# Kernel tuning notes

Hardware: AMD Instinct MI355X
Metric: run time of the kernel (lower is better)

## Reference

```python
import jax, jax.numpy as jnp
import numpy as np

N_NODES = 100000
N_EDGES = 1000000
IN_DIM = 64
HID = 64
OUT = 64
NEG_SLOPE = 0.2  # PyG GATConv default


def setup_inputs() -> dict:
    key = jax.random.key(0)
    ks = jax.random.split(key, 10)
    x = jax.random.normal(ks[0], (N_NODES, IN_DIM), dtype=jnp.float32)
    edge_index = jax.random.randint(ks[1], (2, N_EDGES), 0, N_NODES, dtype=jnp.int64)
    s = 1.0 / np.sqrt(IN_DIM)
    sh = 1.0 / np.sqrt(HID)
    W_src = jax.random.uniform(ks[2], (IN_DIM, HID), jnp.float32, -s, s)
    W_dst = jax.random.uniform(ks[3], (IN_DIM, HID), jnp.float32, -s, s)
    att_src = jax.random.uniform(ks[4], (HID,), jnp.float32, -sh, sh)
    att_dst = jax.random.uniform(ks[5], (HID,), jnp.float32, -sh, sh)
    bias = jnp.zeros((HID,), jnp.float32)
    W_lin = jax.random.uniform(ks[6], (HID, OUT), jnp.float32, -sh, sh)
    b_lin = jax.random.uniform(ks[7], (OUT,), jnp.float32, -sh, sh)
    return {"x": x, "edge_index": edge_index, "W_src": W_src, "W_dst": W_dst,
            "att_src": att_src, "att_dst": att_dst, "bias": bias,
            "W_lin": W_lin, "b_lin": b_lin}


def reference(x, edge_index, W_src, W_dst, att_src, att_dst, bias, W_lin, b_lin):
    src, tgt = edge_index[0], edge_index[1]
    # Bias-free linear projections (PyG GATConv with tuple in_channels)
    h_src = x @ W_src                      # [N, HID]
    h_dst = x @ W_dst                      # [N, HID]
    a_src = h_src @ att_src                # [N]
    a_dst = h_dst @ att_dst                # [N]
    # Per-edge attention logits: LeakyReLU(a_src[j] + a_dst[i])
    e = a_src[src] + a_dst[tgt]            # [E]
    e = jnp.where(e > 0, e, NEG_SLOPE * e)
    # Segment-softmax over incoming edges of each target node
    seg_max = jax.ops.segment_max(e, tgt, num_segments=N_NODES)  # [N]
    expw = jnp.exp(e - seg_max[tgt])                             # [E]
    denom = jax.ops.segment_sum(expw, tgt, num_segments=N_NODES)  # [N]
    alpha = expw / (denom[tgt] + 1e-16)                          # [E]
    # Scatter-aggregate weighted source features
    msgs = alpha[:, None] * h_src[src]                           # [E, HID]
    out = jax.ops.segment_sum(msgs, tgt, num_segments=N_NODES)   # [N, HID]
    out = out + bias
    # Final linear + ReLU
    return jax.nn.relu(out @ W_lin + b_lin)
```

## Files before the change

### kernel.cpp

```cpp
#include <hip/hip_runtime.h>
#include <hip/hip_fp16.h>
#include <math.h>

#define HID 64
#define CBITS 6
#define CSZ 64
#define MAXB 2048
#define CAP 832
#define PB 896
#define MSB 256
#define XSTR 17

__device__ __forceinline__ float4 f4fma(float a, const float4 b, float4 c) {
    c.x = fmaf(a, b.x, c.x); c.y = fmaf(a, b.y, c.y);
    c.z = fmaf(a, b.z, c.z); c.w = fmaf(a, b.w, c.w);
    return c;
}

__global__ void __launch_bounds__(256)
mid_kernel(const float* __restrict__ x,
           const float* __restrict__ W_src,
           const float* __restrict__ W_dst,
           const float* __restrict__ att_src,
           const float* __restrict__ att_dst,
           __half* __restrict__ h_half,
           float* __restrict__ a_src,
           float* __restrict__ a_dst, int N,
           const int* __restrict__ src, const int* __restrict__ tgt,
           int* __restrict__ gcursor, int* __restrict__ rec, int E, int nbc) {
    __shared__ __align__(16) char smraw[25600];
    const int t = threadIdx.x;

    if (blockIdx.x < PB) {
        float4* Ws4  = (float4*)smraw;
        float4* att4 = Ws4 + HID * 16;
        float4* vd4  = att4 + 16;
        float4* xs4f = vd4 + 16;

        for (int i = t; i < HID * 16; i += 256) Ws4[i] = ((const float4*)W_src)[i];
        if (t < 16) att4[t] = ((const float4*)att_src)[t];
        if (t < HID) {
            float acc = 0.0f;
#pragma unroll 8
            for (int h = 0; h < HID; ++h)
                acc = fmaf(W_dst[t * HID + h], att_dst[h], acc);
            ((float*)vd4)[t] = acc;
        }

        const int g0 = t >> 4;
        const int s = t & 15;
        const float4* x4 = (const float4*)x;
        uint2* h2 = (uint2*)h_half;

        for (int base = blockIdx.x * 32; base < N; base += PB * 32) {
            __syncthreads();
#pragma unroll
            for (int u = 0; u < 2; ++u) {
                int f = t + u * 256;
                int node = base + (f >> 4);
                xs4f[(f >> 4) * XSTR + (f & 15)] =
                    (node < N) ? x4[(long long)node * 16 + (f & 15)]
                               : make_float4(0, 0, 0, 0);
            }
            __syncthreads();

            const float4* xr0 = xs4f + g0 * XSTR;
            const float4* xr1 = xs4f + (g0 + 16) * XSTR;

            float4 acc0 = make_float4(0, 0, 0, 0);
            float4 acc1 = make_float4(0, 0, 0, 0);
#pragma unroll 4
            for (int kk = 0; kk < 16; ++kk) {
                float4 xv0 = xr0[kk];
                float4 xv1 = xr1[kk];
                float4 w0 = Ws4[(4 * kk + 0) * 16 + s];
                float4 w1 = Ws4[(4 * kk + 1) * 16 + s];
                float4 w2 = Ws4[(4 * kk + 2) * 16 + s];
                float4 w3 = Ws4[(4 * kk + 3) * 16 + s];
                acc0 = f4fma(xv0.x, w0, acc0);
                acc1 = f4fma(xv1.x, w0, acc1);
                acc0 = f4fma(xv0.y, w1, acc0);
                acc1 = f4fma(xv1.y, w1, acc1);
                acc0 = f4fma(xv0.z, w2, acc0);
                acc1 = f4fma(xv1.z, w2, acc1);
                acc0 = f4fma(xv0.w, w3, acc0);
                acc1 = f4fma(xv1.w, w3, acc1);
            }

            float4 av = att4[s], qv = vd4[s];
            float p0 = acc0.x * av.x + acc0.y * av.y + acc0.z * av.z + acc0.w * av.w;
            float p1 = acc1.x * av.x + acc1.y * av.y + acc1.z * av.z + acc1.w * av.w;
            float4 xq0 = xr0[s];
            float4 xq1 = xr1[s];
            float q0 = xq0.x * qv.x + xq0.y * qv.y + xq0.z * qv.z + xq0.w * qv.w;
            float q1 = xq1.x * qv.x + xq1.y * qv.y + xq1.z * qv.z + xq1.w * qv.w;
#pragma unroll
            for (int off = 1; off < 16; off <<= 1) {
                p0 += __shfl_xor(p0, off, 64);
                p1 += __shfl_xor(p1, off, 64);
                q0 += __shfl_xor(q0, off, 64);
                q1 += __shfl_xor(q1, off, 64);
            }

            int n0 = base + g0, n1 = base + g0 + 16;
            if (n0 < N) {
                __half2 lo = __float22half2_rn(make_float2(acc0.x, acc0.y));
                __half2 hi = __float22half2_rn(make_float2(acc0.z, acc0.w));
                uint2 pk; pk.x = *(unsigned*)&lo; pk.y = *(unsigned*)&hi;
                h2[(long long)n0 * 16 + s] = pk;
                if (s == 0) { a_src[n0] = p0; a_dst[n0] = q0; }
            }
            if (n1 < N) {
                __half2 lo = __float22half2_rn(make_float2(acc1.x, acc1.y));
                __half2 hi = __float22half2_rn(make_float2(acc1.z, acc1.w));
                uint2 pk; pk.x = *(unsigned*)&lo; pk.y = *(unsigned*)&hi;
                h2[(long long)n1 * 16 + s] = pk;
                if (s == 0) { a_src[n1] = p1; a_dst[n1] = q1; }
            }
        }
    } else {
        int* lh = (int*)smraw;
        const int bid = blockIdx.x - PB;

        for (int i = t; i < nbc; i += 256) lh[i] = 0;
        __syncthreads();
        int chunk = (E + MSB - 1) / MSB;
        int e0 = bid * chunk;
        int e1 = min(E, e0 + chunk);
        for (int e = e0 + t; e < e1; e += 256)
            atomicAdd(&lh[tgt[e] >> CBITS], 1);
        __syncthreads();
        for (int i = t; i < nbc; i += 256)
            if (lh[i]) lh[i] = i * CAP + atomicAdd(&gcursor[i], lh[i]);
        __syncthreads();
        for (int e = e0 + t; e < e1; e += 256) {
            int s = src[e], tg = tgt[e];
            int bi = tg >> CBITS;
            int pos = atomicAdd(&lh[bi], 1);
            if (pos < (bi + 1) * CAP)
                rec[pos] = (s << CBITS) | (tg & (CSZ - 1));
        }
    }
}

__global__ void __launch_bounds__(256)
sort_gather_kernel(const int* __restrict__ gcursor, const int* __restrict__ rec,
                   const __half* __restrict__ h_half,
                   const float* __restrict__ a_src, const float* __restrict__ a_dst,
                   const float* __restrict__ bias,
                   const float* __restrict__ W_lin, const float* __restrict__ b_lin,
                   float* __restrict__ out, int N) {
    __shared__ float4 Wl4[HID * 16];
    __shared__ float4 bs4[16], bl4[16];
    __shared__ int ssort[CAP];
    __shared__ int hist[CSZ];
    __shared__ int loff[CSZ + 1];
    __shared__ int cur[CSZ];

    const int t = threadIdx.x;
    for (int i = t; i < HID * 16; i += 256) Wl4[i] = ((const float4*)W_lin)[i];
    if (t < 16) {
        bs4[t] = ((const float4*)bias)[t];
        bl4[t] = ((const float4*)b_lin)[t];
    }

    const int bk = blockIdx.x;
    const int node0 = bk << CBITS;
    const int nn = min(CSZ, N - node0);
    const int beg = bk * CAP;
    int cnt = gcursor[bk];
    if (cnt > CAP) cnt = CAP;

    if (t < CSZ) hist[t] = 0;
    __syncthreads();
    for (int j = t; j < cnt; j += 256)
        atomicAdd(&hist[rec[beg + j] & (CSZ - 1)], 1);
    __syncthreads();
    if (t < CSZ) {
        int h = hist[t];
        int v = h;
#pragma unroll
        for (int off = 1; off < CSZ; off <<= 1) {
            int u = __shfl_up(v, off, 64);
            if (t >= off) v += u;
        }
        loff[t] = v - h;
        cur[t]  = v - h;
        if (t == CSZ - 1) loff[CSZ] = v;
    }
    __syncthreads();
    for (int j = t; j < cnt; j += 256) {
        int r = rec[beg + j];
        int pos = atomicAdd(&cur[r & (CSZ - 1)], 1);
        ssort[pos] = r >> CBITS;
    }
    __syncthreads();

    const int lane = t & 63;
    const int w = t >> 6;
    const int g = lane >> 4;
    const int s = lane & 15;
    const int gbase = g << 4;
    const uint2* h2 = (const uint2*)h_half;
    float4* out4 = (float4*)out;

#pragma unroll 1
    for (int r2 = 0; r2 < 4; ++r2) {
        int nloc = w * 16 + r2 * 4 + g;
        int n = node0 + nloc;
        bool act = (nloc < nn);
        float adn = act ? a_dst[n] : 0.0f;
        int jb = loff[nloc];
        int je = loff[nloc + 1];

        float4 acc = make_float4(0, 0, 0, 0);
        float dsum = 0.0f;
        int j = jb;
        for (; j + 4 <= je; j += 4) {
            int s0 = ssort[j], s1 = ssort[j + 1], s2 = ssort[j + 2], s3 = ssort[j + 3];
            uint2 r0 = h2[(long long)s0 * 16 + s];
            uint2 r1 = h2[(long long)s1 * 16 + s];
            uint2 r2v = h2[(long long)s2 * 16 + s];
            uint2 r3 = h2[(long long)s3 * 16 + s];
            float v0 = a_src[s0] + adn, v1 = a_src[s1] + adn;
            float v2 = a_src[s2] + adn, v3 = a_src[s3] + adn;
            v0 = (v0 > 0.0f) ? v0 : 0.2f * v0;
            v1 = (v1 > 0.0f) ? v1 : 0.2f * v1;
            v2 = (v2 > 0.0f) ? v2 : 0.2f * v2;
            v3 = (v3 > 0.0f) ? v3 : 0.2f * v3;
            float w0 = __expf(v0), w1 = __expf(v1);
            float w2 = __expf(v2), w3 = __expf(v3);
            dsum += (w0 + w1) + (w2 + w3);
            float2 f0a = __half22float2(*(const __half2*)&r0.x);
            float2 f0b = __half22float2(*(const __half2*)&r0.y);
            float2 f1a = __half22float2(*(const __half2*)&r1.x);
            float2 f1b = __half22float2(*(const __half2*)&r1.y);
            float2 f2a = __half22float2(*(const __half2*)&r2v.x);
            float2 f2b = __half22float2(*(const __half2*)&r2v.y);
            float2 f3a = __half22float2(*(const __half2*)&r3.x);
            float2 f3b = __half22float2(*(const __half2*)&r3.y);
            acc.x = fmaf(w0, f0a.x, fmaf(w1, f1a.x, fmaf(w2, f2a.x, fmaf(w3, f3a.x, acc.x))));
            acc.y = fmaf(w0, f0a.y, fmaf(w1, f1a.y, fmaf(w2, f2a.y, fmaf(w3, f3a.y, acc.y))));
            acc.z = fmaf(w0, f0b.x, fmaf(w1, f1b.x, fmaf(w2, f2b.x, fmaf(w3, f3b.x, acc.z))));
            acc.w = fmaf(w0, f0b.y, fmaf(w1, f1b.y, fmaf(w2, f2b.y, fmaf(w3, f3b.y, acc.w))));
        }
        for (; j < je; ++j) {
            int s0 = ssort[j];
            uint2 r0 = h2[(long long)s0 * 16 + s];
            float v0 = a_src[s0] + adn;
            v0 = (v0 > 0.0f) ? v0 : 0.2f * v0;
            float w0 = __expf(v0);
            dsum += w0;
            float2 f0a = __half22float2(*(const __half2*)&r0.x);
            float2 f0b = __half22float2(*(const __half2*)&r0.y);
            acc.x = fmaf(w0, f0a.x, acc.x);
            acc.y = fmaf(w0, f0a.y, acc.y);
            acc.z = fmaf(w0, f0b.x, acc.z);
            acc.w = fmaf(w0, f0b.y, acc.w);
        }

        float inv = 1.0f / (dsum + 1e-16f);
        float4 bsv = bs4[s];
        float4 r;
        r.x = fmaf(acc.x, inv, bsv.x);
        r.y = fmaf(acc.y, inv, bsv.y);
        r.z = fmaf(acc.z, inv, bsv.z);
        r.w = fmaf(acc.w, inv, bsv.w);

        float4 o = bl4[s];
#pragma unroll 4
        for (int ks = 0; ks < 16; ++ks) {
            float rx = __shfl(r.x, gbase + ks, 64);
            float ry = __shfl(r.y, gbase + ks, 64);
            float rz = __shfl(r.z, gbase + ks, 64);
            float rw = __shfl(r.w, gbase + ks, 64);
            o = f4fma(rx, Wl4[(4 * ks + 0) * 16 + s], o);
            o = f4fma(ry, Wl4[(4 * ks + 1) * 16 + s], o);
            o = f4fma(rz, Wl4[(4 * ks + 2) * 16 + s], o);
            o = f4fma(rw, Wl4[(4 * ks + 3) * 16 + s], o);
        }

        if (act) {
            float4 res;
            res.x = o.x > 0.0f ? o.x : 0.0f;
            res.y = o.y > 0.0f ? o.y : 0.0f;
            res.z = o.z > 0.0f ? o.z : 0.0f;
            res.w = o.w > 0.0f ? o.w : 0.0f;
            out4[(long long)n * 16 + s] = res;
        }
    }
}

extern "C" void kernel_launch(void* const* d_in, const int* in_sizes, int n_in,
                              void* d_out, int out_size, void* d_ws, size_t ws_size,
                              hipStream_t stream) {
    const float* x       = (const float*)d_in[0];
    const int*   edge    = (const int*)d_in[1];
    const float* W_src   = (const float*)d_in[2];
    const float* W_dst   = (const float*)d_in[3];
    const float* att_src = (const float*)d_in[4];
    const float* att_dst = (const float*)d_in[5];
    const float* bias    = (const float*)d_in[6];
    const float* W_lin   = (const float*)d_in[7];
    const float* b_lin   = (const float*)d_in[8];
    float* out = (float*)d_out;

    const int N = in_sizes[0] / HID;
    const int E = in_sizes[1] / 2;
    const int* src = edge;
    const int* tgt = edge + E;
    const int nbc = (N + CSZ - 1) / CSZ;

    __half* h_half  = (__half*)d_ws;
    float*  a_src   = (float*)(h_half + (size_t)N * HID);
    float*  a_dst   = a_src + N;
    int*    gcursor = (int*)(a_dst + N);
    int*    rec     = gcursor + MAXB;

    hipMemsetAsync(gcursor, 0, MAXB * sizeof(int), stream);
    mid_kernel<<<PB + MSB, 256, 0, stream>>>(x, W_src, W_dst, att_src, att_dst,
                                             h_half, a_src, a_dst, N,
                                             src, tgt, gcursor, rec, E, nbc);
    sort_gather_kernel<<<nbc, 256, 0, stream>>>(gcursor, rec, h_half, a_src, a_dst,
                                                bias, W_lin, b_lin, out, N);
}
```

Before: 166.9 us.

## Software-pipeline gather loop, keep records in registers, init cursors via kernel

The gather loop now prefetches the next four source rows and attention scores while it computes on the current four, hiding load latency. The bucket records are loaded once into registers and reused for both the histogram and the scatter passes instead of being reread from global memory. Bias vectors move from shared memory into registers, launch bounds request 8 waves' occupancy, and the memset is replaced by a small kernel that seeds each cursor with its bucket base offset. The risks are higher register pressure from the prefetch buffers and a hard-coded cap of four records per thread, which assumes CAP is at most 1024.

Measured after the change: 165.3 us. About the same (-1.0%).

```diff
diff --git a/kernel.cpp b/kernel.cpp
--- a/kernel.cpp
+++ b/kernel.cpp
@@ -15,6 +15,12 @@
     c.x = fmaf(a, b.x, c.x); c.y = fmaf(a, b.y, c.y);
     c.z = fmaf(a, b.z, c.z); c.w = fmaf(a, b.w, c.w);
     return c;
+}
+
+__global__ void init_kernel(int* __restrict__ gcursor, int nbc) {
+    int stride = gridDim.x * blockDim.x;
+    for (int i = blockIdx.x * blockDim.x + threadIdx.x; i < nbc; i += stride)
+        gcursor[i] = i * CAP;
 }
 
 __global__ void __launch_bounds__(256)
@@ -131,7 +137,7 @@
             atomicAdd(&lh[tgt[e] >> CBITS], 1);
         __syncthreads();
         for (int i = t; i < nbc; i += 256)
-            if (lh[i]) lh[i] = i * CAP + atomicAdd(&gcursor[i], lh[i]);
+            if (lh[i]) lh[i] = atomicAdd(&gcursor[i], lh[i]);
         __syncthreads();
         for (int e = e0 + t; e < e1; e += 256) {
             int s = src[e], tg = tgt[e];
@@ -143,7 +149,7 @@
     }
 }
 
-__global__ void __launch_bounds__(256)
+__global__ void __launch_bounds__(256, 8)
 sort_gather_kernel(const int* __restrict__ gcursor, const int* __restrict__ rec,
                    const __half* __restrict__ h_half,
                    const float* __restrict__ a_src, const float* __restrict__ a_dst,
@@ -151,30 +157,31 @@
                    const float* __restrict__ W_lin, const float* __restrict__ b_lin,
                    float* __restrict__ out, int N) {
     __shared__ float4 Wl4[HID * 16];
-    __shared__ float4 bs4[16], bl4[16];
-    __shared__ int ssort[CAP];
-    __shared__ int hist[CSZ];
-    __shared__ int loff[CSZ + 1];
-    __shared__ int cur[CSZ];
+    __shared__ int   ssort[CAP];
+    __shared__ int   loff[CSZ + 1];
+    __shared__ int   hist[CSZ];
 
     const int t = threadIdx.x;
     for (int i = t; i < HID * 16; i += 256) Wl4[i] = ((const float4*)W_lin)[i];
-    if (t < 16) {
-        bs4[t] = ((const float4*)bias)[t];
-        bl4[t] = ((const float4*)b_lin)[t];
-    }
 
     const int bk = blockIdx.x;
     const int node0 = bk << CBITS;
     const int nn = min(CSZ, N - node0);
     const int beg = bk * CAP;
-    int cnt = gcursor[bk];
+    int cnt = gcursor[bk] - beg;
     if (cnt > CAP) cnt = CAP;
 
     if (t < CSZ) hist[t] = 0;
     __syncthreads();
-    for (int j = t; j < cnt; j += 256)
-        atomicAdd(&hist[rec[beg + j] & (CSZ - 1)], 1);
+
+    int q0 = (t       < cnt) ? rec[beg + t      ] : -1;
+    int q1 = (t + 256 < cnt) ? rec[beg + t + 256] : -1;
+    int q2 = (t + 512 < cnt) ? rec[beg + t + 512] : -1;
+    int q3 = (t + 768 < cnt) ? rec[beg + t + 768] : -1;
+    if (q0 >= 0) atomicAdd(&hist[q0 & (CSZ - 1)], 1);
+    if (q1 >= 0) atomicAdd(&hist[q1 & (CSZ - 1)], 1);
+    if (q2 >= 0) atomicAdd(&hist[q2 & (CSZ - 1)], 1);
+    if (q3 >= 0) atomicAdd(&hist[q3 & (CSZ - 1)], 1);
     __syncthreads();
     if (t < CSZ) {
         int h = hist[t];
@@ -185,15 +192,14 @@
             if (t >= off) v += u;
         }
         loff[t] = v - h;
-        cur[t]  = v - h;
+        hist[t] = v - h;
         if (t == CSZ - 1) loff[CSZ] = v;
     }
     __syncthreads();
-    for (int j = t; j < cnt; j += 256) {
-        int r = rec[beg + j];
-        int pos = atomicAdd(&cur[r & (CSZ - 1)], 1);
-        ssort[pos] = r >> CBITS;
-    }
+    if (q0 >= 0) ssort[atomicAdd(&hist[q0 & (CSZ - 1)], 1)] = q0;
+    if (q1 >= 0) ssort[atomicAdd(&hist[q1 & (CSZ - 1)], 1)] = q1;
+    if (q2 >= 0) ssort[atomicAdd(&hist[q2 & (CSZ - 1)], 1)] = q2;
+    if (q3 >= 0) ssort[atomicAdd(&hist[q3 & (CSZ - 1)], 1)] = q3;
     __syncthreads();
 
     const int lane = t & 63;
@@ -203,6 +209,8 @@
     const int gbase = g << 4;
     const uint2* h2 = (const uint2*)h_half;
     float4* out4 = (float4*)out;
+    const float4 bsv = ((const float4*)bias)[s];
+    const float4 blv = ((const float4*)b_lin)[s];
 
 #pragma unroll 1
     for (int r2 = 0; r2 < 4; ++r2) {
@@ -216,14 +224,28 @@
         float4 acc = make_float4(0, 0, 0, 0);
         float dsum = 0.0f;
         int j = jb;
-        for (; j + 4 <= je; j += 4) {
-            int s0 = ssort[j], s1 = ssort[j + 1], s2 = ssort[j + 2], s3 = ssort[j + 3];
-            uint2 r0 = h2[(long long)s0 * 16 + s];
-            uint2 r1 = h2[(long long)s1 * 16 + s];
-            uint2 r2v = h2[(long long)s2 * 16 + s];
-            uint2 r3 = h2[(long long)s3 * 16 + s];
-            float v0 = a_src[s0] + adn, v1 = a_src[s1] + adn;
-            float v2 = a_src[s2] + adn, v3 = a_src[s3] + adn;
+        uint2 pr0 = make_uint2(0, 0), pr1 = pr0, pr2 = pr0, pr3 = pr0;
+        float pa0 = 0.0f, pa1 = 0.0f, pa2 = 0.0f, pa3 = 0.0f;
+        if (j + 4 <= je) {
+            int c0 = ssort[j] >> CBITS,     c1 = ssort[j + 1] >> CBITS;
+            int c2 = ssort[j + 2] >> CBITS, c3 = ssort[j + 3] >> CBITS;
+            pr0 = h2[((unsigned)c0 << 4) + s];
+            pr1 = h2[((unsigned)c1 << 4) + s];
+            pr2 = h2[((unsigned)c2 << 4) + s];
+            pr3 = h2[((unsigned)c3 << 4) + s];
+            pa0 = a_src[c0]; pa1 = a_src[c1]; pa2 = a_src[c2]; pa3 = a_src[c3];
+        }
+#pragma unroll 1
+        for (; j + 8 <= je; j += 4) {
+            int c0 = ssort[j + 4] >> CBITS, c1 = ssort[j + 5] >> CBITS;
+            int c2 = ssort[j + 6] >> CBITS, c3 = ssort[j + 7] >> CBITS;
+            uint2 nr0 = h2[((unsigned)c0 << 4) + s];
+            uint2 nr1 = h2[((unsigned)c1 << 4) + s];
+            uint2 nr2 = h2[((unsigned)c2 << 4) + s];
+            uint2 nr3 = h2[((unsigned)c3 << 4) + s];
+            float na0 = a_src[c0], na1 = a_src[c1];
+            float na2 = a_src[c2], na3 = a_src[c3];
+            float v0 = pa0 + adn, v1 = pa1 + adn, v2 = pa2 + adn, v3 = pa3 + adn;
             v0 = (v0 > 0.0f) ? v0 : 0.2f * v0;
             v1 = (v1 > 0.0f) ? v1 : 0.2f * v1;
             v2 = (v2 > 0.0f) ? v2 : 0.2f * v2;
@@ -231,23 +253,48 @@
             float w0 = __expf(v0), w1 = __expf(v1);
             float w2 = __expf(v2), w3 = __expf(v3);
             dsum += (w0 + w1) + (w2 + w3);
-            float2 f0a = __half22float2(*(const __half2*)&r0.x);
-            float2 f0b = __half22float2(*(const __half2*)&r0.y);
-            float2 f1a = __half22float2(*(const __half2*)&r1.x);
-            float2 f1b = __half22float2(*(const __half2*)&r1.y);
-            float2 f2a = __half22float2(*(const __half2*)&r2v.x);
-            float2 f2b = __half22float2(*(const __half2*)&r2v.y);
-            float2 f3a = __half22float2(*(const __half2*)&r3.x);
-            float2 f3b = __half22float2(*(const __half2*)&r3.y);
+            float2 f0a = __half22float2(*(const __half2*)&pr0.x);
+            float2 f0b = __half22float2(*(const __half2*)&pr0.y);
+            float2 f1a = __half22float2(*(const __half2*)&pr1.x);
+            float2 f1b = __half22float2(*(const __half2*)&pr1.y);
+            float2 f2a = __half22float2(*(const __half2*)&pr2.x);
+            float2 f2b = __half22float2(*(const __half2*)&pr2.y);
+            float2 f3a = __half22float2(*(const __half2*)&pr3.x);
+            float2 f3b = __half22float2(*(const __half2*)&pr3.y);
             acc.x = fmaf(w0, f0a.x, fmaf(w1, f1a.x, fmaf(w2, f2a.x, fmaf(w3, f3a.x, acc.x))));
             acc.y = fmaf(w0, f0a.y, fmaf(w1, f1a.y, fmaf(w2, f2a.y, fmaf(w3, f3a.y, acc.y))));
             acc.z = fmaf(w0, f0b.x, fmaf(w1, f1b.x, fmaf(w2, f2b.x, fmaf(w3, f3b.x, acc.z))));
             acc.w = fmaf(w0, f0b.y, fmaf(w1, f1b.y, fmaf(w2, f2b.y, fmaf(w3, f3b.y, acc.w))));
+            pr0 = nr0; pr1 = nr1; pr2 = nr2; pr3 = nr3;
+            pa0 = na0; pa1 = na1; pa2 = na2; pa3 = na3;
+        }
+        if (j + 4 <= je) {
+            float v0 = pa0 + adn, v1 = pa1 + adn, v2 = pa2 + adn, v3 = pa3 + adn;
+            v0 = (v0 > 0.0f) ? v0 : 0.2f * v0;
+            v1 = (v1 > 0.0f) ? v1 : 0.2f * v1;
+            v2 = (v2 > 0.0f) ? v2 : 0.2f * v2;
+            v3 = (v3 > 0.0f) ? v3 : 0.2f * v3;
+            float w0 = __expf(v0), w1 = __expf(v1);
+            float w2 = __expf(v2), w3 = __expf(v3);
+            dsum += (w0 + w1) + (w2 + w3);
+            float2 f0a = __half22float2(*(const __half2*)&pr0.x);
+            float2 f0b = __half22float2(*(const __half2*)&pr0.y);
+            float2 f1a = __half22float2(*(const __half2*)&pr1.x);
+            float2 f1b = __half22float2(*(const __half2*)&pr1.y);
+            float2 f2a = __half22float2(*(const __half2*)&pr2.x);
+            float2 f2b = __half22float2(*(const __half2*)&pr2.y);
+            float2 f3a = __half22float2(*(const __half2*)&pr3.x);
+            float2 f3b = __half22float2(*(const __half2*)&pr3.y);
+            acc.x = fmaf(w0, f0a.x, fmaf(w1, f1a.x, fmaf(w2, f2a.x, fmaf(w3, f3a.x, acc.x))));
+            acc.y = fmaf(w0, f0a.y, fmaf(w1, f1a.y, fmaf(w2, f2a.y, fmaf(w3, f3a.y, acc.y))));
+            acc.z = fmaf(w0, f0b.x, fmaf(w1, f1b.x, fmaf(w2, f2b.x, fmaf(w3, f3b.x, acc.z))));
+            acc.w = fmaf(w0, f0b.y, fmaf(w1, f1b.y, fmaf(w2, f2b.y, fmaf(w3, f3b.y, acc.w))));
+            j += 4;
         }
         for (; j < je; ++j) {
-            int s0 = ssort[j];
-            uint2 r0 = h2[(long long)s0 * 16 + s];
-            float v0 = a_src[s0] + adn;
+            int c0 = ssort[j] >> CBITS;
+            uint2 r0 = h2[((unsigned)c0 << 4) + s];
+            float v0 = a_src[c0] + adn;
             v0 = (v0 > 0.0f) ? v0 : 0.2f * v0;
             float w0 = __expf(v0);
             dsum += w0;
@@ -260,14 +307,13 @@
         }
 
         float inv = 1.0f / (dsum + 1e-16f);
-        float4 bsv = bs4[s];
         float4 r;
         r.x = fmaf(acc.x, inv, bsv.x);
         r.y = fmaf(acc.y, inv, bsv.y);
         r.z = fmaf(acc.z, inv, bsv.z);
         r.w = fmaf(acc.w, inv, bsv.w);
 
-        float4 o = bl4[s];
+        float4 o = blv;
 #pragma unroll 4
         for (int ks = 0; ks < 16; ++ks) {
             float rx = __shfl(r.x, gbase + ks, 64);
@@ -317,7 +363,7 @@
     int*    gcursor = (int*)(a_dst + N);
     int*    rec     = gcursor + MAXB;
 
-    hipMemsetAsync(gcursor, 0, MAXB * sizeof(int), stream);
+    init_kernel<<<8, 256, 0, stream>>>(gcursor, nbc);
     mid_kernel<<<PB + MSB, 256, 0, stream>>>(x, W_src, W_dst, att_src, att_dst,
                                              h_half, a_src, a_dst, N,
                                              src, tgt, gcursor, rec, E, nbc);
```

## Load x directly from global, precompute W_dst·att_dst in init kernel

Applied to the files above, without the earlier changes.

Replaces the hipMemsetAsync with a small init kernel that computes the W_dst·att_dst vector once and seeds each bucket cursor with its base offset (i*CAP), so the scatter and gather stages no longer add the base themselves. The projection blocks stop staging x tiles in LDS: each thread reads its x rows straight from global memory, which removes two __syncthreads per tile and shrinks shared memory for better occupancy. In exchange, the same x row is re-read by the 16 threads of a group through cache rather than from LDS.

New measurement: 179.3 us. 1.07x slower.

```diff
diff --git a/kernel.cpp b/kernel.cpp
--- a/kernel.cpp
+++ b/kernel.cpp
@@ -9,7 +9,6 @@
 #define CAP 832
 #define PB 896
 #define MSB 256
-#define XSTR 17
 
 __device__ __forceinline__ float4 f4fma(float a, const float4 b, float4 c) {
     c.x = fmaf(a, b.x, c.x); c.y = fmaf(a, b.y, c.y);
@@ -17,62 +16,64 @@
     return c;
 }
 
+__global__ void init_kernel(const float* __restrict__ W_dst,
+                            const float* __restrict__ att_dst,
+                            float* __restrict__ vdst,
+                            int* __restrict__ gcursor, int nbc) {
+    if (blockIdx.x == 0 && threadIdx.x < HID) {
+        int k = threadIdx.x;
+        float acc = 0.0f;
+#pragma unroll 8
+        for (int h = 0; h < HID; ++h) acc = fmaf(W_dst[k * HID + h], att_dst[h], acc);
+        vdst[k] = acc;
+    }
+    int stride = gridDim.x * blockDim.x;
+    for (int i = blockIdx.x * blockDim.x + threadIdx.x; i < nbc; i += stride)
+        gcursor[i] = i * CAP;
+}
+
 __global__ void __launch_bounds__(256)
 mid_kernel(const float* __restrict__ x,
            const float* __restrict__ W_src,
-           const float* __restrict__ W_dst,
            const float* __restrict__ att_src,
-           const float* __restrict__ att_dst,
+           const float* __restrict__ vdst,
            __half* __restrict__ h_half,
            float* __restrict__ a_src,
            float* __restrict__ a_dst, int N,
            const int* __restrict__ src, const int* __restrict__ tgt,
            int* __restrict__ gcursor, int* __restrict__ rec, int E, int nbc) {
-    __shared__ __align__(16) char smraw[25600];
+    __shared__ __align__(16) char smraw[16896];
     const int t = threadIdx.x;
 
     if (blockIdx.x < PB) {
         float4* Ws4  = (float4*)smraw;
         float4* att4 = Ws4 + HID * 16;
         float4* vd4  = att4 + 16;
-        float4* xs4f = vd4 + 16;
 
         for (int i = t; i < HID * 16; i += 256) Ws4[i] = ((const float4*)W_src)[i];
-        if (t < 16) att4[t] = ((const float4*)att_src)[t];
-        if (t < HID) {
-            float acc = 0.0f;
-#pragma unroll 8
-            for (int h = 0; h < HID; ++h)
-                acc = fmaf(W_dst[t * HID + h], att_dst[h], acc);
-            ((float*)vd4)[t] = acc;
-        }
+        if (t < 16) {
+            att4[t] = ((const float4*)att_src)[t];
+            vd4[t]  = ((const float4*)vdst)[t];
+        }
+        __syncthreads();
 
         const int g0 = t >> 4;
         const int s = t & 15;
         const float4* x4 = (const float4*)x;
         uint2* h2 = (uint2*)h_half;
+        const float4 zf4 = make_float4(0, 0, 0, 0);
 
         for (int base = blockIdx.x * 32; base < N; base += PB * 32) {
-            __syncthreads();
-#pragma unroll
-            for (int u = 0; u < 2; ++u) {
-                int f = t + u * 256;
-                int node = base + (f >> 4);
-                xs4f[(f >> 4) * XSTR + (f & 15)] =
-                    (node < N) ? x4[(long long)node * 16 + (f & 15)]
-                               : make_float4(0, 0, 0, 0);
-            }
-            __syncthreads();
-
-            const float4* xr0 = xs4f + g0 * XSTR;
-            const float4* xr1 = xs4f + (g0 + 16) * XSTR;
-
-            float4 acc0 = make_float4(0, 0, 0, 0);
-            float4 acc1 = make_float4(0, 0, 0, 0);
+            const int n0 = base + g0, n1 = base + g0 + 16;
+            const bool a0 = (n0 < N), a1 = (n1 < N);
+            const float4* xp0 = x4 + (long long)n0 * 16;
+            const float4* xp1 = x4 + (long long)n1 * 16;
+
+            float4 acc0 = zf4, acc1 = zf4;
 #pragma unroll 4
             for (int kk = 0; kk < 16; ++kk) {
-                float4 xv0 = xr0[kk];
-                float4 xv1 = xr1[kk];
+                float4 xv0 = a0 ? xp0[kk] : zf4;
+                float4 xv1 = a1 ? xp1[kk] : zf4;
                 float4 w0 = Ws4[(4 * kk + 0) * 16 + s];
                 float4 w1 = Ws4[(4 * kk + 1) * 16 + s];
                 float4 w2 = Ws4[(4 * kk + 2) * 16 + s];
@@ -90,8 +91,8 @@
             float4 av = att4[s], qv = vd4[s];
             float p0 = acc0.x * av.x + acc0.y * av.y + acc0.z * av.z + acc0.w * av.w;
             float p1 = acc1.x * av.x + acc1.y * av.y + acc1.z * av.z + acc1.w * av.w;
-            float4 xq0 = xr0[s];
-            float4 xq1 = xr1[s];
+            float4 xq0 = a0 ? xp0[s] : zf4;
+            float4 xq1 = a1 ? xp1[s] : zf4;
             float q0 = xq0.x * qv.x + xq0.y * qv.y + xq0.z * qv.z + xq0.w * qv.w;
             float q1 = xq1.x * qv.x + xq1.y * qv.y + xq1.z * qv.z + xq1.w * qv.w;
 #pragma unroll
@@ -102,15 +103,14 @@
                 q1 += __shfl_xor(q1, off, 64);
             }
 
-            int n0 = base + g0, n1 = base + g0 + 16;
-            if (n0 < N) {
+            if (a0) {
                 __half2 lo = __float22half2_rn(make_float2(acc0.x, acc0.y));
                 __half2 hi = __float22half2_rn(make_float2(acc0.z, acc0.w));
                 uint2 pk; pk.x = *(unsigned*)&lo; pk.y = *(unsigned*)&hi;
                 h2[(long long)n0 * 16 + s] = pk;
                 if (s == 0) { a_src[n0] = p0; a_dst[n0] = q0; }
             }
-            if (n1 < N) {
+            if (a1) {
                 __half2 lo = __float22half2_rn(make_float2(acc1.x, acc1.y));
                 __half2 hi = __float22half2_rn(make_float2(acc1.z, acc1.w));
                 uint2 pk; pk.x = *(unsigned*)&lo; pk.y = *(unsigned*)&hi;
@@ -131,7 +131,7 @@
             atomicAdd(&lh[tgt[e] >> CBITS], 1);
         __syncthreads();
         for (int i = t; i < nbc; i += 256)
-            if (lh[i]) lh[i] = i * CAP + atomicAdd(&gcursor[i], lh[i]);
+            if (lh[i]) lh[i] = atomicAdd(&gcursor[i], lh[i]);
         __syncthreads();
         for (int e = e0 + t; e < e1; e += 256) {
             int s = src[e], tg = tgt[e];
@@ -168,7 +168,7 @@
     const int node0 = bk << CBITS;
     const int nn = min(CSZ, N - node0);
     const int beg = bk * CAP;
-    int cnt = gcursor[bk];
+    int cnt = gcursor[bk] - beg;
     if (cnt > CAP) cnt = CAP;
 
     if (t < CSZ) hist[t] = 0;
@@ -314,12 +314,13 @@
     __half* h_half  = (__half*)d_ws;
     float*  a_src   = (float*)(h_half + (size_t)N * HID);
     float*  a_dst   = a_src + N;
-    int*    gcursor = (int*)(a_dst + N);
+    float*  vdst    = a_dst + N;
+    int*    gcursor = (int*)(vdst + 64);
     int*    rec     = gcursor + MAXB;
 
-    hipMemsetAsync(gcursor, 0, MAXB * sizeof(int), stream);
-    mid_kernel<<<PB + MSB, 256, 0, stream>>>(x, W_src, W_dst, att_src, att_dst,
-                                             h_half, a_src, a_dst, N,
+    init_kernel<<<8, 256, 0, stream>>>(W_dst, att_dst, vdst, gcursor, nbc);
+    mid_kernel<<<PB + MSB, 256, 0, stream>>>(x, W_src, att_src, vdst, h_half,
+                                             a_src, a_dst, N,
                                              src, tgt, gcursor, rec, E, nbc);
     sort_gather_kernel<<<nbc, 256, 0, stream>>>(gcursor, rec, h_half, a_src, a_dst,
                                                 bias, W_lin, b_lin, out, N);
```
